# Kernel tuning notes

Hardware: AMD Instinct MI355X
Metric: run time of the kernel (lower is better)

Reference implementation:

```python
import jax, jax.numpy as jnp
import numpy as np

# Static config (KITTI PointPillars-style)
B, PB, N = 4, 12000, 32          # batches, pillars per batch, max points per pillar
P = B * PB
NX, NY, NZ, F = 432, 496, 1, 64  # grid and PFN output channels
PX, PY, PZ = 0.16, 0.16, 4.0     # pillar size
XO, YO, ZO = 0.08, -39.6, -1.0   # pillar-center offsets = size/2 + range_min
EPS = 1e-3                        # BatchNorm eps


def setup_inputs() -> dict:
    key = jax.random.key(0)
    ks = jax.random.split(key, 10)
    pillars = jax.random.normal(ks[0], (P, N, 8), jnp.float32)
    # unique BEV cells per batch so the scatter (torch advanced-index assign) is well-defined
    rng = np.random.default_rng(0)
    cs = []
    for b in range(B):
        lin = rng.choice(NY * NX, size=PB, replace=False)
        cs.append(np.stack([np.full(PB, b), np.zeros(PB, np.int64), lin // NX, lin % NX], 1))
    coords = jnp.asarray(np.concatenate(cs, 0), jnp.int32)  # [P,4] = (batch, z, y, x)
    num_points = jax.random.randint(ks[1], (P,), 1, N + 1, jnp.int32)

    def bn_stats(k, f):  # rows: gamma, beta, running_mean, running_var
        k1, k2, k3, k4 = jax.random.split(k, 4)
        return jnp.stack([jax.random.uniform(k1, (f,), jnp.float32, 0.8, 1.2),
                          jax.random.normal(k2, (f,)) * 0.1,
                          jax.random.normal(k3, (f,)) * 0.1,
                          jax.random.uniform(k4, (f,), jnp.float32, 0.5, 1.5)])

    return {
        'pillars': pillars,
        'w1': jax.random.normal(ks[2], (10, F), jnp.float32) * 0.1,
        'bn1': bn_stats(ks[4], F),
        'w2': jax.random.normal(ks[3], (8, F), jnp.float32) * 0.1,
        'bn2': bn_stats(ks[5], F),
        'wf1': jax.random.normal(ks[6], (F,), jnp.float32) * 0.1,
        'wf2': jax.random.normal(ks[7], (F,), jnp.float32) * 0.1,
        'fbn1': bn_stats(ks[8], 1)[:, 0],
        'fbn2': bn_stats(ks[9], 1)[:, 0],
        'coords': coords,
        'num_points': num_points,
    }


def _bn(x, stats):  # x [..., F], stats [4, F] or [4]
    g, b, m, v = stats[0], stats[1], stats[2], stats[3]
    return (x - m) * (g * jax.lax.rsqrt(v + EPS)) + b


def _pfn(x, w, stats):  # x [P, N, C] -> [P, F]: linear + BN(eval) + relu + max over points
    h = jnp.einsum('pnc,cf->pnf', x, w)
    return jax.nn.relu(_bn(h, stats)).max(axis=1)


def _forward(pillars, w1, bn1, w2, bn2, wf1, wf2, fbn1, fbn2, coords, num_points):
    xyz = pillars[:, :, :3]                                   # [P, N, 3]
    # relative xyz to cluster mean
    mean_xyz = xyz.sum(axis=1, keepdims=True) / num_points.astype(jnp.float32)[:, None, None]
    to_cluster = xyz - mean_xyz
    # relative xyz to pillar center; coords cols = (batch, z, y, x)
    cf = coords.astype(jnp.float32)
    center = jnp.stack([cf[:, 3] * PX + XO, cf[:, 2] * PY + YO, cf[:, 1] * PZ + ZO], axis=-1)
    to_center = xyz - center[:, None, :]

    pv_in = jnp.concatenate([pillars[:, :, :4], to_cluster, to_center], axis=-1)  # [P, N, 10]
    f1 = _pfn(pv_in, w1, bn1)      # [P, F] geometric stream
    f2 = _pfn(pillars, w2, bn2)    # [P, F] seg stream (full 8 channels)

    # scatter pillar features to BEV canvas: idx = z + y*nx + x (nz=1 -> z=0)
    lin = coords[:, 1] + coords[:, 2] * NX + coords[:, 3]
    b_idx = coords[:, 0]
    bev1 = jnp.zeros((B, NZ * NY * NX, F), jnp.float32).at[b_idx, lin].set(f1)
    bev2 = jnp.zeros((B, NZ * NY * NX, F), jnp.float32).at[b_idx, lin].set(f2)
    x1 = bev1.reshape(B, NY, NX, F).transpose(0, 3, 1, 2)  # [B, F, NY, NX]
    x2 = bev2.reshape(B, NY, NX, F).transpose(0, 3, 1, 2)

    # attentional fusion: 1x1 conv (no bias) + BN2d(1) per stream, softmax over the 2 weights
    s1 = _bn(jnp.einsum('bfyx,f->byx', x1, wf1), fbn1)
    s2 = _bn(jnp.einsum('bfyx,f->byx', x2, wf2), fbn2)
    aw = jax.nn.softmax(jnp.stack([s1, s2], axis=1), axis=1)  # [B, 2, NY, NX]
    return x1 * aw[:, 0:1] + x2 * aw[:, 1:2]


def reference(pillars, w1, bn1, w2, bn2, wf1, wf2, fbn1, fbn2, coords, num_points):
    return _forward(pillars, w1, bn1, w2, bn2, wf1, wf2, fbn1, fbn2, coords, num_points)
```

## Files before the change

kernel.cpp:

```cpp
#include <hip/hip_runtime.h>
#include <math.h>

#define NXC 432
#define NYC 496
#define CELLS (NYC * NXC)
#define BATCH 4
#define PTOT 48000
#define NPT 32
#define EPSC 1e-3f

__global__ __launch_bounds__(256) void pfe_kernel(
    const float* __restrict__ pillars, const float* __restrict__ w1,
    const float* __restrict__ bn1, const float* __restrict__ w2,
    const float* __restrict__ bn2, const float* __restrict__ wf1,
    const float* __restrict__ wf2, const float* __restrict__ fbn1,
    const float* __restrict__ fbn2, const int* __restrict__ coords,
    const int* __restrict__ num_points, float* __restrict__ comb,
    int* __restrict__ map)
{
    __shared__ float lds[4 * NPT * 8];
    const int tid  = threadIdx.x;
    const int wave = tid >> 6;
    const int lane = tid & 63;
    const int pbase = blockIdx.x * 4;

    {
        const float4* src = (const float4*)(pillars + (size_t)pbase * (NPT * 8));
        ((float4*)lds)[tid] = src[tid];
    }
    __syncthreads();

    const int p = pbase + wave;
    const float* pl = lds + wave * (NPT * 8);

    float sx = 0.f, sy = 0.f, sz = 0.f;
    if (lane < NPT) {
        sx = pl[lane * 8 + 0];
        sy = pl[lane * 8 + 1];
        sz = pl[lane * 8 + 2];
    }
#pragma unroll
    for (int off = 32; off; off >>= 1) {
        sx += __shfl_xor(sx, off);
        sy += __shfl_xor(sy, off);
        sz += __shfl_xor(sz, off);
    }
    const float inv_np = 1.0f / (float)num_points[p];
    const float mxm = sx * inv_np, mym = sy * inv_np, mzm = sz * inv_np;

    const int c1 = coords[p * 4 + 1], c2 = coords[p * 4 + 2], c3 = coords[p * 4 + 3];
    const float cx = c3 * 0.16f + 0.08f;
    const float cy = c2 * 0.16f + (-39.6f);
    const float cz = c1 * 4.0f  + (-1.0f);

    const int f = lane;

    const float g1 = bn1[f], be1 = bn1[64 + f], bm1 = bn1[128 + f], bv1 = bn1[192 + f];
    const float s1 = g1 * rsqrtf(bv1 + EPSC);
    const float w10 = w1[f],        w11 = w1[64 + f],  w12 = w1[128 + f], w13 = w1[192 + f];
    const float w14 = w1[256 + f],  w15 = w1[320 + f], w16 = w1[384 + f];
    const float w17 = w1[448 + f],  w18 = w1[512 + f], w19 = w1[576 + f];
    const float AX = (w10 + w14 + w17) * s1;
    const float AY = (w11 + w15 + w18) * s1;
    const float AZ = (w12 + w16 + w19) * s1;
    const float AI = w13 * s1;
    const float C0 = be1 - bm1 * s1
                   - (mxm * w14 + mym * w15 + mzm * w16) * s1
                   - (cx * w17 + cy * w18 + cz * w19) * s1;

    const float g2 = bn2[f], be2 = bn2[64 + f], bm2 = bn2[128 + f], bv2 = bn2[192 + f];
    const float s2 = g2 * rsqrtf(bv2 + EPSC);
    const float B0 = w2[f] * s2,        B1 = w2[64 + f] * s2;
    const float B2 = w2[128 + f] * s2,  B3 = w2[192 + f] * s2;
    const float B4 = w2[256 + f] * s2,  B5 = w2[320 + f] * s2;
    const float B6 = w2[384 + f] * s2,  B7 = w2[448 + f] * s2;
    const float C2 = be2 - bm2 * s2;

    float max1 = -1e30f, max2 = -1e30f;
#pragma unroll 8
    for (int n = 0; n < NPT; n++) {
        const float4 a  = *(const float4*)(pl + n * 8);
        const float4 q  = *(const float4*)(pl + n * 8 + 4);
        const float h1 = fmaf(a.x, AX, fmaf(a.y, AY, fmaf(a.z, AZ, fmaf(a.w, AI, C0))));
        max1 = fmaxf(max1, h1);
        const float h2 = fmaf(a.x, B0, fmaf(a.y, B1, fmaf(a.z, B2, fmaf(a.w, B3,
                        fmaf(q.x, B4, fmaf(q.y, B5, fmaf(q.z, B6, fmaf(q.w, B7, C2))))))));
        max2 = fmaxf(max2, h2);
    }
    const float f1v = fmaxf(max1, 0.f);
    const float f2v = fmaxf(max2, 0.f);

    float d1 = f1v * wf1[f];
    float d2 = f2v * wf2[f];
#pragma unroll
    for (int off = 32; off; off >>= 1) {
        d1 += __shfl_xor(d1, off);
        d2 += __shfl_xor(d2, off);
    }
    const float sc1 = (d1 - fbn1[2]) * (fbn1[0] * rsqrtf(fbn1[3] + EPSC)) + fbn1[1];
    const float sc2 = (d2 - fbn2[2]) * (fbn2[0] * rsqrtf(fbn2[3] + EPSC)) + fbn2[1];
    const float a0 = 1.0f / (1.0f + expf(sc2 - sc1));

    comb[p * 64 + f] = fmaf(f1v - f2v, a0, f2v);

    if (lane == 0) {
        const int lin  = c1 + c2 * NXC + c3;
        const int bidx = coords[p * 4 + 0];
        map[bidx * CELLS + lin] = p;
    }
}

__global__ __launch_bounds__(256) void emit_kernel(
    const int* __restrict__ map, const float* __restrict__ comb,
    float* __restrict__ out)
{
    const int cell = blockIdx.x * 256 + threadIdx.x;
    const int b = cell / CELLS;
    const int L = cell - b * CELLS;
    const int m = map[cell];

    const float sel = (m < 0) ? 0.f : 1.f;
    const int  mm   = (m < 0) ? 0   : m;
    const float* c  = comb + mm * 64;
    float* o = out + (b * 64) * CELLS + L;

#pragma unroll
    for (int fq = 0; fq < 16; fq++) {
        const float4 v = *(const float4*)(c + fq * 4);
        __builtin_nontemporal_store(v.x * sel, o + (fq * 4 + 0) * CELLS);
        __builtin_nontemporal_store(v.y * sel, o + (fq * 4 + 1) * CELLS);
        __builtin_nontemporal_store(v.z * sel, o + (fq * 4 + 2) * CELLS);
        __builtin_nontemporal_store(v.w * sel, o + (fq * 4 + 3) * CELLS);
    }
}

extern "C" void kernel_launch(void* const* d_in, const int* in_sizes, int n_in,
                              void* d_out, int out_size, void* d_ws, size_t ws_size,
                              hipStream_t stream) {
    const float* pillars = (const float*)d_in[0];
    const float* w1      = (const float*)d_in[1];
    const float* bn1     = (const float*)d_in[2];
    const float* w2      = (const float*)d_in[3];
    const float* bn2     = (const float*)d_in[4];
    const float* wf1     = (const float*)d_in[5];
    const float* wf2     = (const float*)d_in[6];
    const float* fbn1    = (const float*)d_in[7];
    const float* fbn2    = (const float*)d_in[8];
    const int*   coords  = (const int*)d_in[9];
    const int*   nump    = (const int*)d_in[10];
    float* out = (float*)d_out;

    int*   map  = (int*)d_ws;
    float* comb = (float*)((char*)d_ws + (size_t)BATCH * CELLS * 4);

    hipMemsetAsync(map, 0xFF, (size_t)BATCH * CELLS * 4, stream);
    pfe_kernel<<<PTOT / 4, 256, 0, stream>>>(pillars, w1, bn1, w2, bn2,
                                             wf1, wf2, fbn1, fbn2,
                                             coords, nump, comb, map);
    emit_kernel<<<(BATCH * CELLS) / 256, 256, 0, stream>>>(map, comb, out);
}
```

Before: 98.05 us.

## Transpose emit through LDS for vector stores and pack PFN math

The emit kernel now gathers 128 cells' features into a padded shared-memory tile and writes the channel-major output with 16-byte nontemporal vector stores, in place of scalar strided stores. The PFE kernel transposes each pillar's points into channel-major LDS and evaluates the two linear+max streams on float2 vectors, which lets the compiler use packed FMA. The output write is the dominant memory traffic, so wider coalesced stores target the main cost. The price is an extra LDS round trip and a barrier per block, plus a larger LDS footprint per block.

```diff
diff --git a/kernel.cpp b/kernel.cpp
--- a/kernel.cpp
+++ b/kernel.cpp
@@ -8,6 +8,10 @@
 #define PTOT 48000
 #define NPT 32
 #define EPSC 1e-3f
+#define TCELLS 128
+
+typedef float f2 __attribute__((ext_vector_type(2)));
+typedef float f4v __attribute__((ext_vector_type(4)));
 
 __global__ __launch_bounds__(256) void pfe_kernel(
     const float* __restrict__ pillars, const float* __restrict__ w1,
@@ -18,26 +22,33 @@
     const int* __restrict__ num_points, float* __restrict__ comb,
     int* __restrict__ map)
 {
-    __shared__ float lds[4 * NPT * 8];
+    __shared__ float lds[4 * 256];
     const int tid  = threadIdx.x;
     const int wave = tid >> 6;
     const int lane = tid & 63;
     const int pbase = blockIdx.x * 4;
 
     {
-        const float4* src = (const float4*)(pillars + (size_t)pbase * (NPT * 8));
-        ((float4*)lds)[tid] = src[tid];
+        const float4 v = ((const float4*)(pillars + (size_t)pbase * 256))[tid];
+        const int w  = tid >> 6;
+        const int n  = (tid & 63) >> 1;
+        const int c0 = (tid & 1) * 4;
+        float* dst = lds + w * 256 + n;
+        dst[(c0 + 0) * 32] = v.x;
+        dst[(c0 + 1) * 32] = v.y;
+        dst[(c0 + 2) * 32] = v.z;
+        dst[(c0 + 3) * 32] = v.w;
     }
     __syncthreads();
 
     const int p = pbase + wave;
-    const float* pl = lds + wave * (NPT * 8);
+    const float* pl = lds + wave * 256;
 
     float sx = 0.f, sy = 0.f, sz = 0.f;
-    if (lane < NPT) {
-        sx = pl[lane * 8 + 0];
-        sy = pl[lane * 8 + 1];
-        sz = pl[lane * 8 + 2];
+    if (lane < 32) {
+        sx = pl[lane];
+        sy = pl[32 + lane];
+        sz = pl[64 + lane];
     }
 #pragma unroll
     for (int off = 32; off; off >>= 1) {
@@ -70,25 +81,58 @@
 
     const float g2 = bn2[f], be2 = bn2[64 + f], bm2 = bn2[128 + f], bv2 = bn2[192 + f];
     const float s2 = g2 * rsqrtf(bv2 + EPSC);
-    const float B0 = w2[f] * s2,        B1 = w2[64 + f] * s2;
-    const float B2 = w2[128 + f] * s2,  B3 = w2[192 + f] * s2;
-    const float B4 = w2[256 + f] * s2,  B5 = w2[320 + f] * s2;
-    const float B6 = w2[384 + f] * s2,  B7 = w2[448 + f] * s2;
+    const float b0 = w2[f] * s2,        b1 = w2[64 + f] * s2;
+    const float b2 = w2[128 + f] * s2,  b3 = w2[192 + f] * s2;
+    const float b4 = w2[256 + f] * s2,  b5 = w2[320 + f] * s2;
+    const float b6 = w2[384 + f] * s2,  b7 = w2[448 + f] * s2;
     const float C2 = be2 - bm2 * s2;
 
-    float max1 = -1e30f, max2 = -1e30f;
-#pragma unroll 8
-    for (int n = 0; n < NPT; n++) {
-        const float4 a  = *(const float4*)(pl + n * 8);
-        const float4 q  = *(const float4*)(pl + n * 8 + 4);
-        const float h1 = fmaf(a.x, AX, fmaf(a.y, AY, fmaf(a.z, AZ, fmaf(a.w, AI, C0))));
-        max1 = fmaxf(max1, h1);
-        const float h2 = fmaf(a.x, B0, fmaf(a.y, B1, fmaf(a.z, B2, fmaf(a.w, B3,
-                        fmaf(q.x, B4, fmaf(q.y, B5, fmaf(q.z, B6, fmaf(q.w, B7, C2))))))));
-        max2 = fmaxf(max2, h2);
-    }
-    const float f1v = fmaxf(max1, 0.f);
-    const float f2v = fmaxf(max2, 0.f);
+    const f2 AX2 = {AX, AX}, AY2 = {AY, AY}, AZ2 = {AZ, AZ}, AI2 = {AI, AI};
+    const f2 B02 = {b0, b0}, B12 = {b1, b1}, B22 = {b2, b2}, B32 = {b3, b3};
+    const f2 B42 = {b4, b4}, B52 = {b5, b5}, B62 = {b6, b6}, B72 = {b7, b7};
+    const f2 C02 = {C0, C0}, C22 = {C2, C2};
+
+    f2 m1 = {-1e30f, -1e30f}, m2 = {-1e30f, -1e30f};
+#pragma unroll
+    for (int k = 0; k < 8; k++) {
+        const float4 X = *(const float4*)(pl + 0 * 32 + 4 * k);
+        const float4 Y = *(const float4*)(pl + 1 * 32 + 4 * k);
+        const float4 Z = *(const float4*)(pl + 2 * 32 + 4 * k);
+        const float4 W = *(const float4*)(pl + 3 * 32 + 4 * k);
+        const float4 Q4 = *(const float4*)(pl + 4 * 32 + 4 * k);
+        const float4 Q5 = *(const float4*)(pl + 5 * 32 + 4 * k);
+        const float4 Q6 = *(const float4*)(pl + 6 * 32 + 4 * k);
+        const float4 Q7 = *(const float4*)(pl + 7 * 32 + 4 * k);
+
+        const f2 xa = {X.x, X.y}, xb = {X.z, X.w};
+        const f2 ya = {Y.x, Y.y}, yb = {Y.z, Y.w};
+        const f2 za = {Z.x, Z.y}, zb = {Z.z, Z.w};
+        const f2 wa = {W.x, W.y}, wb = {W.z, W.w};
+        const f2 qa4 = {Q4.x, Q4.y}, qb4 = {Q4.z, Q4.w};
+        const f2 qa5 = {Q5.x, Q5.y}, qb5 = {Q5.z, Q5.w};
+        const f2 qa6 = {Q6.x, Q6.y}, qb6 = {Q6.z, Q6.w};
+        const f2 qa7 = {Q7.x, Q7.y}, qb7 = {Q7.z, Q7.w};
+
+        f2 h1a = xa * AX2 + C02;  h1a = ya * AY2 + h1a;
+        h1a = za * AZ2 + h1a;     h1a = wa * AI2 + h1a;
+        m1 = __builtin_elementwise_max(m1, h1a);
+        f2 h1b = xb * AX2 + C02;  h1b = yb * AY2 + h1b;
+        h1b = zb * AZ2 + h1b;     h1b = wb * AI2 + h1b;
+        m1 = __builtin_elementwise_max(m1, h1b);
+
+        f2 h2a = xa * B02 + C22;  h2a = ya * B12 + h2a;
+        h2a = za * B22 + h2a;     h2a = wa * B32 + h2a;
+        h2a = qa4 * B42 + h2a;    h2a = qa5 * B52 + h2a;
+        h2a = qa6 * B62 + h2a;    h2a = qa7 * B72 + h2a;
+        m2 = __builtin_elementwise_max(m2, h2a);
+        f2 h2b = xb * B02 + C22;  h2b = yb * B12 + h2b;
+        h2b = zb * B22 + h2b;     h2b = wb * B32 + h2b;
+        h2b = qb4 * B42 + h2b;    h2b = qb5 * B52 + h2b;
+        h2b = qb6 * B62 + h2b;    h2b = qb7 * B72 + h2b;
+        m2 = __builtin_elementwise_max(m2, h2b);
+    }
+    const float f1v = fmaxf(fmaxf(m1.x, m1.y), 0.f);
+    const float f2v = fmaxf(fmaxf(m2.x, m2.y), 0.f);
 
     float d1 = f1v * wf1[f];
     float d2 = f2v * wf2[f];
@@ -114,23 +158,38 @@
     const int* __restrict__ map, const float* __restrict__ comb,
     float* __restrict__ out)
 {
-    const int cell = blockIdx.x * 256 + threadIdx.x;
-    const int b = cell / CELLS;
-    const int L = cell - b * CELLS;
-    const int m = map[cell];
-
-    const float sel = (m < 0) ? 0.f : 1.f;
-    const int  mm   = (m < 0) ? 0   : m;
-    const float* c  = comb + mm * 64;
-    float* o = out + (b * 64) * CELLS + L;
-
-#pragma unroll
-    for (int fq = 0; fq < 16; fq++) {
-        const float4 v = *(const float4*)(c + fq * 4);
-        __builtin_nontemporal_store(v.x * sel, o + (fq * 4 + 0) * CELLS);
-        __builtin_nontemporal_store(v.y * sel, o + (fq * 4 + 1) * CELLS);
-        __builtin_nontemporal_store(v.z * sel, o + (fq * 4 + 2) * CELLS);
-        __builtin_nontemporal_store(v.w * sel, o + (fq * 4 + 3) * CELLS);
+    __shared__ float lds[64 * 132];
+    const int t = threadIdx.x;
+    const int gbase = blockIdx.x * TCELLS;
+
+    {
+        const int c = t >> 1;
+        const int h = (t & 1) * 32;
+        const int m = map[gbase + c];
+        const float sel = (m < 0) ? 0.f : 1.f;
+        const float* src = comb + (size_t)((m < 0) ? 0 : m) * 64 + h;
+        float* dst = lds + h * 132 + c;
+#pragma unroll
+        for (int j = 0; j < 8; j++) {
+            const float4 v = *(const float4*)(src + j * 4);
+            dst[(j * 4 + 0) * 132] = v.x * sel;
+            dst[(j * 4 + 1) * 132] = v.y * sel;
+            dst[(j * 4 + 2) * 132] = v.z * sel;
+            dst[(j * 4 + 3) * 132] = v.w * sel;
+        }
+    }
+    __syncthreads();
+
+    const int b = gbase / CELLS;
+    const int L = gbase - b * CELLS;
+    float* obase = out + (size_t)(b * 64) * CELLS + L;
+#pragma unroll
+    for (int r = 0; r < 8; r++) {
+        const int idx = r * 256 + t;
+        const int f = idx >> 5;
+        const int g = idx & 31;
+        const f4v v = *(const f4v*)(lds + f * 132 + g * 4);
+        __builtin_nontemporal_store(v, (f4v*)(obase + (size_t)f * CELLS + g * 4));
     }
 }
 
@@ -153,9 +212,9 @@
     int*   map  = (int*)d_ws;
     float* comb = (float*)((char*)d_ws + (size_t)BATCH * CELLS * 4);
 
-    hipMemsetAsync(map, 0xFF, (size_t)BATCH * CELLS * 4, stream);
+    (void)hipMemsetAsync(map, 0xFF, (size_t)BATCH * CELLS * 4, stream);
     pfe_kernel<<<PTOT / 4, 256, 0, stream>>>(pillars, w1, bn1, w2, bn2,
                                              wf1, wf2, fbn1, fbn2,
                                              coords, nump, comb, map);
-    emit_kernel<<<(BATCH * CELLS) / 256, 256, 0, stream>>>(map, comb, out);
+    emit_kernel<<<(BATCH * CELLS) / TCELLS, 256, 0, stream>>>(map, comb, out);
 }
```

After: 104.7 us. 6.8% more time.
